# Optimization experiments

Measured on AMD Instinct MI355X. Metric: run time of the kernel, lower is better.

The kernel has to match this reference:

```python
import jax, jax.numpy as jnp
import numpy as np

W_PULL = 1.0
W_PUSH = 1.0
W_NORM = 0.001
W_EDGE = 10.0
DELTA_V = 0.5
DELTA_D = 1.5
CE_W = 1.0
DICE_W = 1.0
IGN = -100
NUM_CLASSES = 8
EMBED_DIM = 16
NUM_INST = 16  # instance ids 1..16, 0 = background
EPS_C = 1e-8
EPS_D = 1e-5


def setup_inputs() -> dict:
    key = jax.random.key(0)
    k1, k2, k3, k4 = jax.random.split(key, 4)
    B, D, H, W = 2, 64, 128, 128
    return {
        "sem_logits": jax.random.normal(k1, (B, NUM_CLASSES, D, H, W), jnp.float32),
        "instance_embed": jax.random.normal(k2, (B, EMBED_DIM, D, H, W), jnp.float32),
        "class_labels": jax.random.randint(k3, (B, D, H, W), 0, NUM_CLASSES, dtype=jnp.int32),
        "labels": jax.random.randint(k4, (B, D, H, W), 0, NUM_INST + 1, dtype=jnp.int32),
    }


def _ce_loss(logits, target):
    # nn.CrossEntropyLoss(ignore_index=-100), mean over valid voxels
    logp = jax.nn.log_softmax(logits, axis=1)
    valid = (target != IGN)
    t_safe = jnp.where(valid, target, 0)
    nll = -jnp.take_along_axis(logp, t_safe[:, None].astype(jnp.int32), axis=1)[:, 0]
    v = valid.astype(logits.dtype)
    return (nll * v).sum() / jnp.maximum(v.sum(), 1.0)


def _dice_loss(logits, target):
    C = logits.shape[1]
    probs = jax.nn.softmax(logits, axis=1)
    valid = (target != IGN)
    t_safe = jnp.where(valid, target, 0)
    one_hot = jax.nn.one_hot(t_safe, C, dtype=probs.dtype, axis=1)  # [B,C,D,H,W]
    vm = valid[:, None].astype(probs.dtype)
    probs = probs * vm
    one_hot = one_hot * vm
    axes = tuple(range(2, probs.ndim))
    inter = (probs * one_hot).sum(axes)
    card_p = probs.sum(axes)
    card_g = one_hot.sum(axes)
    dice = (2.0 * inter + EPS_D) / (card_p + card_g + EPS_D)
    return 1.0 - dice.mean()


def _boundary_weight(labels):
    # morphological gradient: 3x3x3 max-pool minus min-pool, replicate pad
    lf = labels.astype(jnp.float32)
    p = jnp.pad(lf, ((0, 0), (1, 1), (1, 1), (1, 1)), mode='edge')
    mx = jax.lax.reduce_window(p, -jnp.inf, jax.lax.max, (1, 3, 3, 3), (1, 1, 1, 1), 'VALID')
    mn = jax.lax.reduce_window(p, jnp.inf, jax.lax.min, (1, 3, 3, 3), (1, 1, 1, 1), 'VALID')
    boundary = (mx != mn).astype(jnp.float32)
    return 1.0 + boundary * (W_EDGE - 1.0)


def _instance_loss(embed, labels, w):
    B, C = embed.shape[:2]
    e_flat = embed.reshape(B, C, -1)   # [B,C,N]
    l_flat = labels.reshape(B, -1)     # [B,N]
    w_flat = w.reshape(B, -1)          # [B,N] (w_bone == 1 since weight_bone==1.0)
    K = NUM_INST

    def per_batch(e, l, wv):
        seg = lambda x: jax.ops.segment_sum(x, l, num_segments=K + 1)
        wsum = seg(wv)                       # [K+1]
        cnt = seg(jnp.ones_like(wv))         # [K+1]
        cnum = seg((e * wv).T)               # [K+1, C]
        centers = cnum / (wsum[:, None] + EPS_C)
        cg = centers[l]                      # [N, C] gather own-instance center
        dist = jnp.linalg.norm(e.T - cg, axis=-1)
        pull_sum = seg(jax.nn.relu(dist - DELTA_V) ** 2 * wv)
        present = cnt[1:] > 0                # ids 1..K
        loss_pull = jnp.where(present, pull_sum[1:] / jnp.maximum(cnt[1:], 1.0), 0.0).sum()
        c = centers[1:]                      # [K, C]
        iu, ju = jnp.triu_indices(K, k=1)
        pw = jnp.linalg.norm(c[iu] - c[ju], axis=-1)
        pv = (present[iu] & present[ju]).astype(pw.dtype)
        npres = present.sum().astype(pw.dtype)
        npairs = npres * (npres - 1.0) / 2.0
        push = jax.nn.relu(2.0 * DELTA_D - pw) ** 2 * pv
        loss_push = jnp.where(npairs > 0, push.sum() / jnp.maximum(npairs, 1.0), 0.0)
        cn = jnp.linalg.norm(c, axis=-1)
        loss_norm = jnp.where(npres > 0, (cn * present).sum() / jnp.maximum(npres, 1.0), 0.0)
        return loss_pull, loss_push, loss_norm, (npres > 0).astype(jnp.float32)

    lp, lpu, ln, val = jax.vmap(per_batch)(e_flat, l_flat, w_flat)
    n = jnp.maximum(val.sum(), 1.0)
    return (W_PULL * lp.sum() + W_PUSH * lpu.sum() + W_NORM * ln.sum()) / n


def reference(sem_logits, instance_embed, class_labels, labels):
    loss_ce = _ce_loss(sem_logits, class_labels)
    loss_dice = _dice_loss(sem_logits, class_labels)
    loss_sem = CE_W * loss_ce + DICE_W * loss_dice
    w_edge = _boundary_weight(labels)
    # weight_bone == 1.0 -> w_bone = ones (scipy EDT branch disabled by module guard)
    loss_ins = _instance_loss(instance_embed, labels, w_edge)
    loss = loss_sem + loss_ins
    return loss, loss_sem, loss_ce, loss_dice, loss_ins
```

## Files before the change

### kernel.cpp

```cpp
#include <hip/hip_runtime.h>

#define DHW (64*128*128)
#define MIR 32

#define OFF_CEM   0
#define OFF_SEGM  1568
#define OFF_PULLM 21152
#define OFF_CTR   22240
#define OFF_CNT   22784
#define ACC_FLOATS 22818
#define OFF_EDGE_BYTES 92160

typedef __bf16 bf16x8 __attribute__((ext_vector_type(8)));
typedef float f32x4 __attribute__((ext_vector_type(4)));
union FragU { short s[8]; bf16x8 v; };

__device__ inline short f2bf(float f) {
    union { float f; unsigned u; } v; v.f = f;
    unsigned r = v.u + 0x7FFF + ((v.u >> 16) & 1);
    return (short)(r >> 16);
}

__global__ void zero_kernel(float* acc) {
    int i = blockIdx.x * 1024 + threadIdx.x;
    if (i < ACC_FLOATS) acc[i] = 0.0f;
}

__device__ void ce_role(const float* __restrict__ logits, const int* __restrict__ cls,
                        float* __restrict__ acc, int b, int blk, float* sh) {
    int tid = threadIdx.x;
    int mir = blk & (MIR - 1);
    int vb = (blk * 256 + tid) * 4;
    const float* lg = logits + (size_t)b * 8 * DHW;
    const int* cl = cls + (size_t)b * DHW;

    float4 xc[8];
#pragma unroll
    for (int c = 0; c < 8; ++c)
        xc[c] = *reinterpret_cast<const float4*>(&lg[(size_t)c * DHW + vb]);
    int4 t4 = *reinterpret_cast<const int4*>(&cl[vb]);
    int tt[4] = {t4.x, t4.y, t4.z, t4.w};

    float nll = 0.f, cardp[8], inter[8], cardg[8];
#pragma unroll
    for (int c = 0; c < 8; ++c) { cardp[c] = 0.f; inter[c] = 0.f; cardg[c] = 0.f; }

#pragma unroll
    for (int j = 0; j < 4; ++j) {
        float x[8];
#pragma unroll
        for (int c = 0; c < 8; ++c) x[c] = ((const float*)&xc[c])[j];
        int t = tt[j];
        bool valid = (t != -100);
        float mx = x[0];
#pragma unroll
        for (int c = 1; c < 8; ++c) mx = fmaxf(mx, x[c]);
        float e[8], s = 0.f;
#pragma unroll
        for (int c = 0; c < 8; ++c) { e[c] = __expf(x[c] - mx); s += e[c]; }
        float inv = 1.0f / s;
        float lse = __logf(s);
        if (valid) {
#pragma unroll
            for (int c = 0; c < 8; ++c) {
                float p = e[c] * inv;
                cardp[c] += p;
                if (t == c) { inter[c] += p; cardg[c] += 1.f; nll += mx + lse - x[c]; }
            }
        }
    }

    if (tid < 25) sh[tid] = 0.f;
    __syncthreads();
    int lane = tid & 63;
    float vals[25];
    vals[0] = nll;
#pragma unroll
    for (int c = 0; c < 8; ++c) { vals[1 + c] = cardp[c]; vals[9 + c] = inter[c]; vals[17 + c] = cardg[c]; }
#pragma unroll
    for (int i = 0; i < 25; ++i) {
        float r = vals[i];
#pragma unroll
        for (int off = 32; off > 0; off >>= 1) r += __shfl_down(r, off, 64);
        if (lane == 0) atomicAdd(&sh[i], r);
    }
    __syncthreads();
    if (tid < 25) {
        int dst;
        if (tid == 0) dst = 0;
        else if (tid < 9) dst = 1 + b * 8 + (tid - 1);
        else if (tid < 17) dst = 17 + b * 8 + (tid - 9);
        else dst = 33 + b * 8 + (tid - 17);
        atomicAdd(&acc[OFF_CEM + mir * 49 + dst], sh[tid]);
    }
}

__global__ __launch_bounds__(256) void phaseA_kernel(const float* __restrict__ logits,
                                                     const float* __restrict__ embed,
                                                     const int* __restrict__ cls,
                                                     const int* __restrict__ labels,
                                                     float* __restrict__ acc) {
    __shared__ int s_tile[3840];
    __shared__ unsigned char s_eb[256];
    __shared__ float s_cacc[288];
    int x = blockIdx.x;
    int g = x / 11, r3 = x % 11;
    int tid = threadIdx.x;

    if (r3 >= 8) {
        int ce_idx = g * 3 + (r3 - 8);
        int b = (ce_idx >= 384) ? 1 : 0;
        int blk = ce_idx - b * 384;
        ce_role(logits, cls, acc, b, blk, s_cacc);
        return;
    }
    int seg_idx = g * 8 + r3;
    int b = seg_idx & 1;
    int blk = seg_idx >> 1;
    int mir = blk & (MIR - 1);
    int lane = tid & 63;
    int wv = tid >> 6;
    int m = lane & 15;
    int quad = lane >> 4;

    const int* L = labels + (size_t)b * DHW;
    const float* E = embed + (size_t)b * 16 * DHW + (size_t)m * DHW;

    int vb0 = blk * 1024;
    int z0 = vb0 >> 14;
    int y0 = (vb0 >> 7) & 127;

    for (int idx = tid; idx < 960; idx += 256) {
        int row = idx >> 5, col = idx & 31;
        int zi = row / 10, ri = row - zi * 10;
        int zz = min(max(z0 + zi - 1, 0), 63);
        int yy = min(max(y0 + ri - 1, 0), 127);
        reinterpret_cast<int4*>(s_tile)[row * 32 + col] =
            *reinterpret_cast<const int4*>(&L[(zz << 14) + (yy << 7) + col * 4]);
    }
    __syncthreads();

    {
        int p = tid * 4;
        int xx = p & 127, lr = p >> 7;
        int xm = max(xx - 1, 0), xp = min(xx + 4, 127);
        const int* crow = &s_tile[(10 + lr + 1) * 128];
        int4 c; c.x = crow[xx]; c.y = crow[xx + 1]; c.z = crow[xx + 2]; c.w = crow[xx + 3];
        unsigned b0 = 0, b1 = 0, b2 = 0, b3 = 0;
#pragma unroll
        for (int zi = 0; zi < 3; ++zi) {
#pragma unroll
            for (int dy = 0; dy < 3; ++dy) {
                const int* row = &s_tile[(zi * 10 + lr + dy) * 128];
                int rx = row[xx], ry = row[xx + 1], rz = row[xx + 2], rw = row[xx + 3];
                int rm = row[xm], rp = row[xp];
                b0 |= (rm != c.x) | (rx != c.x) | (ry != c.x);
                b1 |= (rx != c.y) | (ry != c.y) | (rz != c.y);
                b2 |= (ry != c.z) | (rz != c.z) | (rw != c.z);
                b3 |= (rz != c.w) | (rw != c.w) | (rp != c.w);
            }
        }
        unsigned eb_own = b0 | (b1 << 1) | (b2 << 2) | (b3 << 3);
        s_eb[tid] = (unsigned char)eb_own;
        unsigned char* EB = (unsigned char*)acc + OFF_EDGE_BYTES + ((size_t)b << 18);
        EB[blk * 256 + tid] = (unsigned char)eb_own;
    }
    __syncthreads();

    int lo0 = wv * 256 + quad * 8;

    f32x4 acc_c = {0.f, 0.f, 0.f, 0.f};
    f32x4 acc_w = {0.f, 0.f, 0.f, 0.f};
    f32x4 acc_n = {0.f, 0.f, 0.f, 0.f};

    FragU ones_col;
#pragma unroll
    for (int j = 0; j < 8; ++j) ones_col.s[j] = (m == 0) ? (short)0x3F80 : (short)0;

    int goff = vb0 + lo0;
    float4 Fa0 = *reinterpret_cast<const float4*>(&E[goff]);
    float4 Fa1 = *reinterpret_cast<const float4*>(&E[goff + 4]);
    float4 Fb0 = *reinterpret_cast<const float4*>(&E[goff + 32]);
    float4 Fb1 = *reinterpret_cast<const float4*>(&E[goff + 36]);

#pragma unroll
    for (int i = 0; i < 8; ++i) {
        float4 cf0, cf1;
        if (i & 1) { cf0 = Fb0; cf1 = Fb1; }
        else       { cf0 = Fa0; cf1 = Fa1; }
        if (i < 6) {
            int noff = goff + (i + 2) * 32;
            if (i & 1) {
                Fb0 = *reinterpret_cast<const float4*>(&E[noff]);
                Fb1 = *reinterpret_cast<const float4*>(&E[noff + 4]);
            } else {
                Fa0 = *reinterpret_cast<const float4*>(&E[noff]);
                Fa1 = *reinterpret_cast<const float4*>(&E[noff + 4]);
            }
        }
        int lo = lo0 + i * 32;
        const int* rowp = &s_tile[(10 + (lo >> 7) + 1) * 128 + (lo & 127)];
        int s0 = i * 8 + quad * 2;
        unsigned short u = *reinterpret_cast<const unsigned short*>(&s_eb[wv * 64 + s0]);
        unsigned eb = (u & 0xF) | ((u >> 4) & 0xF0);

        FragU a, a2, bf;
#pragma unroll
        for (int j = 0; j < 8; ++j) {
            short w = ((eb >> j) & 1) ? (short)0x4120 : (short)0x3F80;
            bool hit = (rowp[j] == m + 1);
            a.s[j]  = hit ? w : (short)0;
            a2.s[j] = hit ? (short)0x3F80 : (short)0;
            float fv = (j < 4) ? ((const float*)&cf0)[j] : ((const float*)&cf1)[j - 4];
            bf.s[j] = f2bf(fv);
        }
        acc_c = __builtin_amdgcn_mfma_f32_16x16x32_bf16(a.v, bf.v, acc_c, 0, 0, 0);
        acc_w = __builtin_amdgcn_mfma_f32_16x16x32_bf16(a.v, ones_col.v, acc_w, 0, 0, 0);
        acc_n = __builtin_amdgcn_mfma_f32_16x16x32_bf16(a2.v, ones_col.v, acc_n, 0, 0, 0);
    }

    for (int i = tid; i < 288; i += 256) s_cacc[i] = 0.f;
    __syncthreads();
#pragma unroll
    for (int rr = 0; rr < 4; ++rr)
        atomicAdd(&s_cacc[(quad * 4 + rr) * 16 + m], acc_c[rr]);
    if (m == 0) {
#pragma unroll
        for (int rr = 0; rr < 4; ++rr) {
            atomicAdd(&s_cacc[256 + quad * 4 + rr], acc_w[rr]);
            atomicAdd(&s_cacc[272 + quad * 4 + rr], acc_n[rr]);
        }
    }
    __syncthreads();
    {
        float* segbase = acc + OFF_SEGM + mir * 612 + b * 306;
        atomicAdd(&segbase[16 + tid], s_cacc[tid]);
        if (tid < 16) atomicAdd(&segbase[272 + 1 + tid], s_cacc[256 + tid]);
        else if (tid < 32) atomicAdd(&segbase[289 + 1 + (tid - 16)], s_cacc[256 + tid]);
    }
}

__global__ __launch_bounds__(1024) void centers_kernel(float* acc) {
    int tid = threadIdx.x;
    if (tid < 544) {
        int b = tid / 272, r = tid % 272;
        int k = r >> 4;
        float cn = 0.f, ws = 0.f;
        for (int mv = 0; mv < MIR; ++mv) {
            const float* segbase = acc + OFF_SEGM + mv * 612 + b * 306;
            if (r >= 16) cn += segbase[r];
            ws += segbase[272 + k];
        }
        acc[OFF_CTR + tid] = (r >= 16) ? cn / (ws + 1e-8f) : 0.f;
    } else if (tid < 578) {
        int j = tid - 544;
        int b = j / 17, k = j % 17;
        float s = 0.f;
        for (int mv = 0; mv < MIR; ++mv)
            s += acc[OFF_SEGM + mv * 612 + b * 306 + 289 + k];
        acc[OFF_CNT + j] = s;
    }
}

__global__ __launch_bounds__(256) void phaseB_kernel(const float* __restrict__ logits,
                                                     const float* __restrict__ embed,
                                                     const int* __restrict__ cls,
                                                     const int* __restrict__ labels,
                                                     float* __restrict__ acc) {
    __shared__ float smem[352];
    int x = blockIdx.x;
    int g = x / 13, r3 = x % 13;
    int tid = threadIdx.x;

    if (r3 >= 8) {
        int ce_idx = g * 5 + (r3 - 8);
        int b = (ce_idx >= 640) ? 1 : 0;
        int blk = 384 + (ce_idx - b * 640);
        ce_role(logits, cls, acc, b, blk, smem);
        return;
    }
    int pull_idx = g * 8 + r3;
    int b = pull_idx & 1;
    int blk = pull_idx >> 1;
    int wv = tid >> 6;
    float* ctr = smem;
    float* ps = smem + 272;
    for (int i = tid; i < 272; i += 256) ctr[i] = acc[OFF_CTR + b * 272 + i];
    for (int i = tid; i < 80; i += 256) ps[i] = 0.f;
    __syncthreads();

    const int* L = labels + (size_t)b * DHW;
    const float* E = embed + (size_t)b * 16 * DHW;
    int vb = (blk * 256 + tid) * 4;

    int4 l4 = *reinterpret_cast<const int4*>(&L[vb]);
    int l[4] = {l4.x, l4.y, l4.z, l4.w};
    unsigned eb;
    {
        const unsigned char* EB = (const unsigned char*)acc + OFF_EDGE_BYTES + ((size_t)b << 18);
        eb = EB[blk * 256 + tid];
    }

    float4 ev[16];
#pragma unroll
    for (int c = 0; c < 16; ++c)
        ev[c] = *reinterpret_cast<const float4*>(&E[(size_t)c * DHW + vb]);

    float d2a[4] = {0.f, 0.f, 0.f, 0.f};
#pragma unroll
    for (int q = 0; q < 4; ++q) {
#pragma unroll
        for (int j = 0; j < 4; ++j) {
            if (l[j] != 0) {
                float4 cv = *reinterpret_cast<const float4*>(&ctr[l[j] * 16 + q * 4]);
                float d0 = ((const float*)&ev[4 * q + 0])[j] - cv.x;
                float d1 = ((const float*)&ev[4 * q + 1])[j] - cv.y;
                float d2 = ((const float*)&ev[4 * q + 2])[j] - cv.z;
                float d3 = ((const float*)&ev[4 * q + 3])[j] - cv.w;
                d2a[j] += d0 * d0 + d1 * d1 + d2 * d2 + d3 * d3;
            }
        }
    }

#pragma unroll
    for (int j = 0; j < 4; ++j) {
        if (l[j] != 0) {
            float w = ((eb >> j) & 1) ? 10.f : 1.f;
            float d = fmaxf(sqrtf(d2a[j]) - 0.5f, 0.f);
            atomicAdd(&ps[wv * 20 + l[j]], d * d * w);
        }
    }
    __syncthreads();
    if (tid >= 1 && tid < 17) {
        float v = ps[tid] + ps[20 + tid] + ps[40 + tid] + ps[60 + tid];
        int mir = blk & (MIR - 1);
        if (v != 0.f) atomicAdd(&acc[OFF_PULLM + mir * 34 + b * 17 + tid], v);
    }
}

__global__ __launch_bounds__(256) void finalize_kernel(const float* __restrict__ acc, float* __restrict__ out) {
    __shared__ float s_ce[49], s_pl[34];
    __shared__ float sh_push[2], sh_norm[2], sh_pull[2], sh_npres[2];
    int tid = threadIdx.x;
    if (tid < 49) {
        float s = 0.f;
        for (int mv = 0; mv < MIR; ++mv) s += acc[OFF_CEM + mv * 49 + tid];
        s_ce[tid] = s;
    }
    if (tid >= 64 && tid < 98) {
        int j = tid - 64;
        float s = 0.f;
        for (int mv = 0; mv < MIR; ++mv) s += acc[OFF_PULLM + mv * 34 + j];
        s_pl[j] = s;
    }
    if (tid < 2) { sh_push[tid] = 0.f; sh_norm[tid] = 0.f; sh_pull[tid] = 0.f; sh_npres[tid] = 0.f; }
    __syncthreads();

    if (tid < 32) {
        int b = tid >> 4, k = (tid & 15) + 1;
        float cnt = acc[OFF_CNT + b * 17 + k];
        if (cnt > 0.f) {
            atomicAdd(&sh_npres[b], 1.f);
            atomicAdd(&sh_pull[b], s_pl[b * 17 + k] / fmaxf(cnt, 1.f));
            const float* c = &acc[OFF_CTR + (b * 17 + k) * 16];
            float n2 = 0.f;
            for (int i = 0; i < 16; ++i) n2 += c[i] * c[i];
            atomicAdd(&sh_norm[b], sqrtf(n2));
        }
    }
    for (int t = tid; t < 240; t += blockDim.x) {
        int b = t / 120, p = t % 120;
        int i = 1, rem = p;
        while (rem >= (16 - i)) { rem -= (16 - i); ++i; }
        int j = i + 1 + rem;
        bool pi = acc[OFF_CNT + b * 17 + i] > 0.f;
        bool pj = acc[OFF_CNT + b * 17 + j] > 0.f;
        if (pi && pj) {
            const float* ci = &acc[OFF_CTR + (b * 17 + i) * 16];
            const float* cj = &acc[OFF_CTR + (b * 17 + j) * 16];
            float d2 = 0.f;
            for (int c = 0; c < 16; ++c) { float dd = ci[c] - cj[c]; d2 += dd * dd; }
            float r = fmaxf(3.0f - sqrtf(d2), 0.f);
            atomicAdd(&sh_push[b], r * r);
        }
    }
    __syncthreads();
    if (tid == 0) {
        float nll = s_ce[0];
        float vcnt = 0.f;
        for (int i = 0; i < 16; ++i) vcnt += s_ce[33 + i];
        float ce = nll / fmaxf(vcnt, 1.f);
        float dsum = 0.f;
        for (int i = 0; i < 16; ++i) {
            float it = s_ce[17 + i], cp = s_ce[1 + i], cg = s_ce[33 + i];
            dsum += (2.f * it + 1e-5f) / (cp + cg + 1e-5f);
        }
        float dice = 1.f - dsum / 16.f;
        float lp = 0.f, lpu = 0.f, ln = 0.f, val = 0.f;
        for (int b = 0; b < 2; ++b) {
            float npres = sh_npres[b];
            lp += sh_pull[b];
            float npairs = npres * (npres - 1.f) * 0.5f;
            lpu += (npairs > 0.f) ? sh_push[b] / fmaxf(npairs, 1.f) : 0.f;
            ln += (npres > 0.f) ? sh_norm[b] / fmaxf(npres, 1.f) : 0.f;
            val += (npres > 0.f) ? 1.f : 0.f;
        }
        float n = fmaxf(val, 1.f);
        float ins = (1.0f * lp + 1.0f * lpu + 0.001f * ln) / n;
        float sem = ce + dice;
        out[0] = sem + ins;
        out[1] = sem;
        out[2] = ce;
        out[3] = dice;
        out[4] = ins;
    }
}

extern "C" void kernel_launch(void* const* d_in, const int* in_sizes, int n_in,
                              void* d_out, int out_size, void* d_ws, size_t ws_size,
                              hipStream_t stream) {
    const float* sem = (const float*)d_in[0];
    const float* emb = (const float*)d_in[1];
    const int* cls = (const int*)d_in[2];
    const int* lab = (const int*)d_in[3];
    float* out = (float*)d_out;
    float* acc = (float*)d_ws;

    hipLaunchKernelGGL(zero_kernel, dim3(23), dim3(1024), 0, stream, acc);
    hipLaunchKernelGGL(phaseA_kernel, dim3(2816), dim3(256), 0, stream, sem, emb, cls, lab, acc);
    hipLaunchKernelGGL(centers_kernel, dim3(1), dim3(1024), 0, stream, acc);
    hipLaunchKernelGGL(phaseB_kernel, dim3(3328), dim3(256), 0, stream, sem, emb, cls, lab, acc);
    hipLaunchKernelGGL(finalize_kernel, dim3(1), dim3(256), 0, stream, acc, out);
}
```

Before: 306.6 us.

## Store per-block segment partials and reduce them in a parallel centers kernel

Phase A blocks now write their per-block segment sums (embedding sums, weights, counts) to a dedicated workspace slot with plain stores instead of atomically adding into mirrored accumulators. A new 34-block centers kernel reduces these partials per (batch, instance) pair and computes the centers and counts. This targets global atomic contention and the single-block centers kernel. The cost is extra workspace traffic and a larger workspace requirement, with a fallback to the old path when the workspace is too small.

```diff
diff --git a/kernel.cpp b/kernel.cpp
--- a/kernel.cpp
+++ b/kernel.cpp
@@ -10,6 +10,7 @@
 #define OFF_CNT   22784
 #define ACC_FLOATS 22818
 #define OFF_EDGE_BYTES 92160
+#define OFF_SEGRAW 160000
 
 typedef __bf16 bf16x8 __attribute__((ext_vector_type(8)));
 typedef float f32x4 __attribute__((ext_vector_type(4)));
@@ -95,6 +96,7 @@
     }
 }
 
+template<int STORE>
 __global__ __launch_bounds__(256) void phaseA_kernel(const float* __restrict__ logits,
                                                      const float* __restrict__ embed,
                                                      const int* __restrict__ cls,
@@ -232,12 +234,52 @@
         }
     }
     __syncthreads();
-    {
+    if (STORE) {
+        float* segp = acc + OFF_SEGRAW + (size_t)seg_idx * 288;
+        segp[tid] = s_cacc[tid];
+        if (tid < 32) segp[256 + tid] = s_cacc[256 + tid];
+    } else {
         float* segbase = acc + OFF_SEGM + mir * 612 + b * 306;
         atomicAdd(&segbase[16 + tid], s_cacc[tid]);
         if (tid < 16) atomicAdd(&segbase[272 + 1 + tid], s_cacc[256 + tid]);
         else if (tid < 32) atomicAdd(&segbase[289 + 1 + (tid - 16)], s_cacc[256 + tid]);
     }
+}
+
+__global__ __launch_bounds__(256) void centers_raw_kernel(float* acc) {
+    int j = blockIdx.x;
+    int b = j / 17, k = j % 17;
+    int tid = threadIdx.x;
+    if (k == 0) {
+        if (tid < 16) acc[OFF_CTR + b * 272 + tid] = 0.f;
+        if (tid == 16) acc[OFF_CNT + b * 17] = 0.f;
+        return;
+    }
+    float vals[18];
+#pragma unroll
+    for (int i = 0; i < 18; ++i) vals[i] = 0.f;
+    for (int t = tid; t < 1024; t += 256) {
+        const float* sp = acc + OFF_SEGRAW + (size_t)(2 * t + b) * 288;
+        const float* row = sp + (k - 1) * 16;
+#pragma unroll
+        for (int c = 0; c < 16; ++c) vals[c] += row[c];
+        vals[16] += sp[256 + (k - 1)];
+        vals[17] += sp[272 + (k - 1)];
+    }
+    __shared__ float sh[18];
+    if (tid < 18) sh[tid] = 0.f;
+    __syncthreads();
+    int lane = tid & 63;
+#pragma unroll
+    for (int i = 0; i < 18; ++i) {
+        float r = vals[i];
+#pragma unroll
+        for (int off = 32; off > 0; off >>= 1) r += __shfl_down(r, off, 64);
+        if (lane == 0) atomicAdd(&sh[i], r);
+    }
+    __syncthreads();
+    if (tid < 16) acc[OFF_CTR + b * 272 + k * 16 + tid] = sh[tid] / (sh[16] + 1e-8f);
+    if (tid == 16) acc[OFF_CNT + b * 17 + k] = sh[17];
 }
 
 __global__ __launch_bounds__(1024) void centers_kernel(float* acc) {
@@ -426,9 +468,17 @@
     float* out = (float*)d_out;
     float* acc = (float*)d_ws;
 
+    size_t need = ((size_t)OFF_SEGRAW + 2048ull * 288ull) * 4ull;
+    bool store_path = (ws_size >= need);
+
     hipLaunchKernelGGL(zero_kernel, dim3(23), dim3(1024), 0, stream, acc);
-    hipLaunchKernelGGL(phaseA_kernel, dim3(2816), dim3(256), 0, stream, sem, emb, cls, lab, acc);
-    hipLaunchKernelGGL(centers_kernel, dim3(1), dim3(1024), 0, stream, acc);
+    if (store_path) {
+        hipLaunchKernelGGL((phaseA_kernel<1>), dim3(2816), dim3(256), 0, stream, sem, emb, cls, lab, acc);
+        hipLaunchKernelGGL(centers_raw_kernel, dim3(34), dim3(256), 0, stream, acc);
+    } else {
+        hipLaunchKernelGGL((phaseA_kernel<0>), dim3(2816), dim3(256), 0, stream, sem, emb, cls, lab, acc);
+        hipLaunchKernelGGL(centers_kernel, dim3(1), dim3(1024), 0, stream, acc);
+    }
     hipLaunchKernelGGL(phaseB_kernel, dim3(3328), dim3(256), 0, stream, sem, emb, cls, lab, acc);
     hipLaunchKernelGGL(finalize_kernel, dim3(1), dim3(256), 0, stream, acc, out);
 }
```

Result: no change. 306.3 us (-0.1%).
